# Optimization experiments

Hardware: AMD Instinct MI355X
Metric: run time of the kernel (lower is better)

## Reference

```python
import jax, jax.numpy as jnp
import numpy as np

N_INPUT, N_HIDDEN, N_OUTPUT = 64, 1024, 64
B, T = 128, 512

def setup_inputs() -> dict:
    key = jax.random.key(0)
    ks = jax.random.split(key, 8)
    s_in = 1.0 / np.sqrt(N_INPUT)
    s_h = 1.0 / np.sqrt(N_HIDDEN)
    return {
        "x": jax.random.normal(ks[0], (B, T, N_INPUT), jnp.float32),
        "enc_w": jax.random.uniform(ks[1], (N_HIDDEN, N_INPUT), jnp.float32, -s_in, s_in),
        "enc_b": jax.random.uniform(ks[2], (N_HIDDEN,), jnp.float32, -s_in, s_in),
        "rec_w": jax.random.uniform(ks[3], (N_HIDDEN, N_HIDDEN), jnp.float32, -s_h, s_h),
        "fgt_w": jax.random.uniform(ks[4], (N_HIDDEN, N_HIDDEN), jnp.float32, -s_h, s_h),
        "dec_w": jax.random.uniform(ks[5], (N_OUTPUT, N_HIDDEN), jnp.float32, -s_h, s_h),
        "dec_b": jax.random.uniform(ks[6], (N_OUTPUT,), jnp.float32, -s_h, s_h),
        "hinit_w": jax.random.uniform(ks[7], (N_HIDDEN, 1), jnp.float32, -1.0, 1.0),
        "hinit_b": jax.random.uniform(jax.random.fold_in(key, 9), (N_HIDDEN,), jnp.float32, -1.0, 1.0),
    }

def softsign(x):
    return x / (1.0 + jnp.abs(x))

def reference(x, enc_w, enc_b, rec_w, fgt_w, dec_w, dec_b, hinit_w, hinit_b):
    # x: [B, T, I] -> time-major [T, B, I]
    xt = jnp.transpose(x, (1, 0, 2))
    # hidden_init(ones(B,1)) = ones @ hinit_w^T + b = broadcast of column sum
    hidden0 = jnp.broadcast_to(hinit_w[:, 0] + hinit_b, (x.shape[0], hinit_b.shape[0]))
    # Precompute encoder projection for all timesteps (same math, one big GEMM)
    enc_all = jnp.einsum('tbi,hi->tbh', xt, enc_w) + enc_b  # [T, B, H]

    def step(hidden, enc_t):
        forget = jax.nn.sigmoid(hidden @ fgt_w.T)
        hidden_new = softsign(enc_t + hidden @ rec_w.T)
        hidden = (1.0 - forget) * hidden + forget * hidden_new
        out_t = hidden @ dec_w.T + dec_b
        return hidden, out_t

    hidden, output = jax.lax.scan(step, hidden0, enc_all)
    return output, hidden  # output: [T, B, O], hidden: [B, H]
```

## Files before the change

### kernel.cpp

```cpp
#include <hip/hip_runtime.h>

typedef unsigned short u16;

#define NWG 256
#define NT  256
#define TS  512
#define HD  1024
#define BS  128
#define NI  64
#define NO  64
#define XR  16
#define CC  32
#define RCP 17

typedef __attribute__((ext_vector_type(8))) short bf16x8;
typedef __attribute__((ext_vector_type(4))) float f32x4;

__device__ __forceinline__ float bf2f(u16 u) {
    union { unsigned int i; float f; } v; v.i = ((unsigned int)u) << 16; return v.f;
}
__device__ __forceinline__ u16 f2bf(float f) {
    union { float fl; unsigned int i; } v; v.fl = f;
    unsigned int x = v.i;
    return (u16)((x + 0x7fffu + ((x >> 16) & 1u)) >> 16);
}
__device__ __forceinline__ float ldv(const void* p, size_t i, bool isf32) {
    return isf32 ? ((const float*)p)[i] : bf2f(((const u16*)p)[i]);
}

__device__ __forceinline__ unsigned l2_atomic_add(unsigned* p, unsigned v) {
    unsigned old;
    asm volatile("global_atomic_add %0, %1, %2, off sc0\n\t"
                 "s_waitcnt vmcnt(0)"
                 : "=&v"(old) : "v"(p), "v"(v) : "memory");
    return old;
}
__device__ __forceinline__ void l2_atomic_swap_nr(unsigned* p, unsigned v) {
    asm volatile("global_atomic_swap %0, %1, off" :: "v"(p), "v"(v) : "memory");
}

__device__ __forceinline__ void load_a_frags(const u16* ap, bf16x8* a) {
    asm volatile(
        "global_load_dwordx4 %0, %8, off sc0\n\t"
        "global_load_dwordx4 %1, %8, off offset:64 sc0\n\t"
        "global_load_dwordx4 %2, %8, off offset:128 sc0\n\t"
        "global_load_dwordx4 %3, %8, off offset:192 sc0\n\t"
        "global_load_dwordx4 %4, %8, off offset:256 sc0\n\t"
        "global_load_dwordx4 %5, %8, off offset:320 sc0\n\t"
        "global_load_dwordx4 %6, %8, off offset:384 sc0\n\t"
        "global_load_dwordx4 %7, %8, off offset:448 sc0\n\t"
        "s_waitcnt vmcnt(0)"
        : "=&v"(a[0]), "=&v"(a[1]), "=&v"(a[2]), "=&v"(a[3]),
          "=&v"(a[4]), "=&v"(a[5]), "=&v"(a[6]), "=&v"(a[7])
        : "v"(ap) : "memory");
}

#define MBL 16

__global__ __launch_bounds__(NT)
void arnn_xcd(const void* __restrict__ xv,
              const void* __restrict__ encwv,
              const void* __restrict__ encbv,
              const void* __restrict__ recwv,
              const void* __restrict__ fgtwv,
              const void* __restrict__ decwv,
              const void* __restrict__ decbv,
              const void* __restrict__ hinitwv,
              const void* __restrict__ hinitbv,
              void* __restrict__ outv,
              u16* __restrict__ h0buf,
              u16* __restrict__ h1buf,
              unsigned* __restrict__ tickets,
              unsigned* __restrict__ mboxes)
{
    __shared__ short WB[132 * 64 * 8];
    __shared__ float redC[4 * 5 * 16 * RCP];
    __shared__ unsigned s_xcd, s_slot;
    __shared__ int s_f32;

    const int tid  = threadIdx.x;
    const int wave = tid >> 6;
    const int lane = tid & 63;
    const int m    = lane & 15;
    const int quad = lane >> 4;

    if (tid == 0) {
        unsigned xcc;
        asm volatile("s_getreg_b32 %0, hwreg(HW_REG_XCC_ID, 0, 4)" : "=s"(xcc));
        xcc &= 7u;
        unsigned slot = l2_atomic_add(tickets + xcc * 16, 1u);
        s_xcd = xcc;
        s_slot = slot & 31u;
        s_f32 = 0;
    }
    __syncthreads();
    {
        float v = bf2f(((const u16*)recwv)[tid]);
        if (!(v >= -1.0f && v <= 1.0f)) s_f32 = 1;
    }
    __syncthreads();
    const bool isf32 = (s_f32 != 0);
    const int xcd  = (int)s_xcd;
    const int slot = (int)s_slot;
    const int b0   = xcd * XR;
    const int j0   = slot * CC;
    const int dt   = slot & 3;
    const int rg   = slot >> 2;
    unsigned* mbX   = mboxes + (size_t)xcd * 32 * 4 * MBL;
    unsigned* mbW   = mbX + (slot * 4 + wave) * MBL;
    const int pw = (slot >> 3), pi = (slot & 7);

    for (int idx = tid; idx < 132 * 64; idx += NT) {
        int ksg = idx >> 6, l = idx & 63, n = l & 15, q = l >> 4;
        int tile, ksl;
        if (ksg < 34)       { tile = 0; ksl = ksg; }
        else if (ksg < 68)  { tile = 1; ksl = ksg - 34; }
        else if (ksg < 100) { tile = 2; ksl = ksg - 68; }
        else                { tile = 3; ksl = ksg - 100; }
        int j = j0 + ((tile & 1) << 4) + n;
        bf16x8 v;
        if (!isf32) {
            const u16* src;
            if (tile < 2) src = (ksl < 32) ? (const u16*)recwv + (size_t)j * HD + ksl * 32 + q * 8
                                           : (const u16*)encwv + (size_t)j * NI + (ksl - 32) * 32 + q * 8;
            else          src = (const u16*)fgtwv + (size_t)j * HD + ksl * 32 + q * 8;
            v = *(const bf16x8*)src;
        } else {
            const float* src;
            if (tile < 2) src = (ksl < 32) ? (const float*)recwv + (size_t)j * HD + ksl * 32 + q * 8
                                           : (const float*)encwv + (size_t)j * NI + (ksl - 32) * 32 + q * 8;
            else          src = (const float*)fgtwv + (size_t)j * HD + ksl * 32 + q * 8;
            #pragma unroll
            for (int i = 0; i < 8; ++i) v[i] = (short)f2bf(src[i]);
        }
        *(bf16x8*)&WB[idx * 8] = v;
    }
    __syncthreads();

    bf16x8 Breg[2][8];
    bf16x8 Freg[2][8];
    #pragma unroll
    for (int ks = 0; ks < 8; ++ks) {
        int kb = wave * 8 + ks;
        Breg[0][ks] = *(const bf16x8*)&WB[((0   + kb) * 64 + lane) * 8];
        Breg[1][ks] = *(const bf16x8*)&WB[((34  + kb) * 64 + lane) * 8];
        Freg[0][ks] = *(const bf16x8*)&WB[((68  + kb) * 64 + lane) * 8];
        Freg[1][ks] = *(const bf16x8*)&WB[((100 + kb) * 64 + lane) * 8];
    }
    bf16x8 Ereg[2];
    if (wave < 2) {
        Ereg[0] = *(const bf16x8*)&WB[((32 + wave) * 64 + lane) * 8];
        Ereg[1] = *(const bf16x8*)&WB[((34 + 32 + wave) * 64 + lane) * 8];
    }
    bf16x8 dfr[8];
    {
        int o = 16 * dt + m;
        #pragma unroll
        for (int ks = 0; ks < 8; ++ks) {
            int kb = wave * 256 + ks * 32 + quad * 8;
            if (!isf32) dfr[ks] = *(const bf16x8*)((const u16*)decwv + (size_t)o * HD + kb);
            else {
                const float* src = (const float*)decwv + (size_t)o * HD + kb;
                #pragma unroll
                for (int i = 0; i < 8; ++i) dfr[ks][i] = (short)f2bf(src[i]);
            }
        }
    }
    const int er2 = tid >> 4, ec2 = (tid & 15) * 2;
    float encb0 = ldv(encbv, j0 + ec2,     isf32);
    float encb1 = ldv(encbv, j0 + ec2 + 1, isf32);
    float decb_r = ldv(decbv, 16 * dt + (tid & 15), isf32);
    float hstA = ldv(hinitwv, j0 + ec2,     isf32) + ldv(hinitbv, j0 + ec2,     isf32);
    float hstB = ldv(hinitwv, j0 + ec2 + 1, isf32) + ldv(hinitbv, j0 + ec2 + 1, isf32);
    {
        unsigned pack = (unsigned)f2bf(hstA) | ((unsigned)f2bf(hstB) << 16);
        *(unsigned*)&h0buf[(size_t)(b0 + er2) * HD + j0 + ec2] = pack;
    }
    __syncthreads();
    if (tid < 32)
        l2_atomic_swap_nr(mbX + (tid * 4 + pw) * MBL + pi, 1u);

    bf16x8 xpB = {};
    f32x4 xr0 = {}, xr1 = {};
    if (wave < 2) {
        size_t xb = (size_t)(b0 + m) * (TS * NI) + (size_t)0 * NI + wave * 32 + quad * 8;
        if (!isf32) xpB = *(const bf16x8*)((const u16*)xv + xb);
        else { const float* xp = (const float*)xv + xb;
               xr0 = *(const f32x4*)xp; xr1 = *(const f32x4*)(xp + 4); }
    }

    for (int t = 0; t < TS; ++t) {
        f32x4 acc[5];
        #pragma unroll
        for (int tt = 0; tt < 5; ++tt) acc[tt] = (f32x4){0.f, 0.f, 0.f, 0.f};

        if (wave < 2) {
            bf16x8 xf;
            if (!isf32) xf = xpB;
            else {
                #pragma unroll
                for (int i = 0; i < 4; ++i) {
                    xf[i]     = (short)f2bf(xr0[i]);
                    xf[i + 4] = (short)f2bf(xr1[i]);
                }
            }
            acc[0] = __builtin_amdgcn_mfma_f32_16x16x32_bf16(xf, Ereg[0], acc[0], 0, 0, 0);
            acc[1] = __builtin_amdgcn_mfma_f32_16x16x32_bf16(xf, Ereg[1], acc[1], 0, 0, 0);
        }

        {
            const unsigned target = (unsigned)(t + 1);
            for (;;) {
                unsigned v = target;
                if (lane < 8) v = l2_atomic_add(mbW + lane, 0u);
                if (__all((int)(v >= target))) break;
            }
        }

        const u16* cur = (t & 1) ? h1buf : h0buf;
        u16*       nxt = (t & 1) ? h0buf : h1buf;

        bf16x8 a[8];
        load_a_frags(cur + (size_t)(b0 + m) * HD + wave * 256 + quad * 8, a);

        if (wave < 2) {
            int tn = (t + 1 < TS) ? t + 1 : t;
            size_t xb = (size_t)(b0 + m) * (TS * NI) + (size_t)tn * NI + wave * 32 + quad * 8;
            if (!isf32) xpB = *(const bf16x8*)((const u16*)xv + xb);
            else { const float* xp = (const float*)xv + xb;
                   xr0 = *(const f32x4*)xp; xr1 = *(const f32x4*)(xp + 4); }
        }

        #pragma unroll
        for (int ks = 0; ks < 8; ++ks) {
            acc[0] = __builtin_amdgcn_mfma_f32_16x16x32_bf16(a[ks], Breg[0][ks], acc[0], 0, 0, 0);
            acc[1] = __builtin_amdgcn_mfma_f32_16x16x32_bf16(a[ks], Breg[1][ks], acc[1], 0, 0, 0);
            acc[2] = __builtin_amdgcn_mfma_f32_16x16x32_bf16(a[ks], Freg[0][ks], acc[2], 0, 0, 0);
            acc[3] = __builtin_amdgcn_mfma_f32_16x16x32_bf16(a[ks], Freg[1][ks], acc[3], 0, 0, 0);
            acc[4] = __builtin_amdgcn_mfma_f32_16x16x32_bf16(a[ks], dfr[ks],     acc[4], 0, 0, 0);
        }

        #pragma unroll
        for (int tt = 0; tt < 5; ++tt) {
            #pragma unroll
            for (int r = 0; r < 4; ++r)
                redC[((wave * 5 + tt) * 16 + quad * 4 + r) * RCP + m] = acc[tt][r];
        }
        __syncthreads();

        {
            const int tl = ec2 >> 4, c0 = ec2 & 15;
            float pr0 = encb0, pf0 = 0.f, pr1 = encb1, pf1 = 0.f;
            #pragma unroll
            for (int kq = 0; kq < 4; ++kq) {
                pr0 += redC[((kq * 5 + tl) * 16 + er2) * RCP + c0];
                pf0 += redC[((kq * 5 + 2 + tl) * 16 + er2) * RCP + c0];
                pr1 += redC[((kq * 5 + tl) * 16 + er2) * RCP + c0 + 1];
                pf1 += redC[((kq * 5 + 2 + tl) * 16 + er2) * RCP + c0 + 1];
            }
            float fg0 = 1.0f / (1.0f + __expf(-pf0));
            float hn0 = pr0 / (1.0f + fabsf(pr0));
            hstA = hstA + fg0 * (hn0 - hstA);
            float fg1 = 1.0f / (1.0f + __expf(-pf1));
            float hn1 = pr1 / (1.0f + fabsf(pr1));
            hstB = hstB + fg1 * (hn1 - hstB);
            unsigned pack = (unsigned)f2bf(hstA) | ((unsigned)f2bf(hstB) << 16);
            *(unsigned*)&nxt[(size_t)(b0 + er2) * HD + j0 + ec2] = pack;
        }
        float dec_o = 0.f;
        int dr = 0;
        if (tid < 32) {
            dr = 2 * rg + (tid >> 4);
            int col = tid & 15;
            dec_o = decb_r;
            #pragma unroll
            for (int kq = 0; kq < 4; ++kq)
                dec_o += redC[((kq * 5 + 4) * 16 + dr) * RCP + col];
        }
        __syncthreads();
        if (tid < 32)
            l2_atomic_swap_nr(mbX + (tid * 4 + pw) * MBL + pi, (unsigned)(t + 2));
        if (tid < 32 && t > 0) {
            size_t oi = (size_t)(t - 1) * (BS * NO) + (size_t)(b0 + dr) * NO + 16 * dt + (tid & 15);
            if (isf32) ((float*)outv)[oi] = dec_o; else ((u16*)outv)[oi] = f2bf(dec_o);
        }
    }

    {
        {
            const unsigned target = (unsigned)(TS + 1);
            for (;;) {
                unsigned v = target;
                if (lane < 8) v = l2_atomic_add(mbW + lane, 0u);
                if (__all((int)(v >= target))) break;
            }
        }
        bf16x8 a[8];
        load_a_frags(h0buf + (size_t)(b0 + m) * HD + wave * 256 + quad * 8, a);
        f32x4 ac = (f32x4){0.f, 0.f, 0.f, 0.f};
        #pragma unroll
        for (int ks = 0; ks < 8; ++ks)
            ac = __builtin_amdgcn_mfma_f32_16x16x32_bf16(a[ks], dfr[ks], ac, 0, 0, 0);
        #pragma unroll
        for (int r = 0; r < 4; ++r)
            redC[((wave * 5 + 4) * 16 + quad * 4 + r) * RCP + m] = ac[r];
        __syncthreads();
        if (tid < 32) {
            int dr = 2 * rg + (tid >> 4), col = tid & 15;
            float o = decb_r;
            #pragma unroll
            for (int kq = 0; kq < 4; ++kq)
                o += redC[((kq * 5 + 4) * 16 + dr) * RCP + col];
            size_t oi = (size_t)511 * (BS * NO) + (size_t)(b0 + dr) * NO + 16 * dt + col;
            if (isf32) ((float*)outv)[oi] = o; else ((u16*)outv)[oi] = f2bf(o);
        }
    }
    {
        size_t oi = (size_t)TS * BS * NO + (size_t)(b0 + er2) * HD + j0 + ec2;
        if (isf32) { ((float*)outv)[oi] = hstA; ((float*)outv)[oi + 1] = hstB; }
        else {
            unsigned pack = (unsigned)f2bf(hstA) | ((unsigned)f2bf(hstB) << 16);
            *(unsigned*)&((u16*)outv)[oi] = pack;
        }
    }
}

extern "C" void kernel_launch(void* const* d_in, const int* in_sizes, int n_in,
                              void* d_out, int out_size, void* d_ws, size_t ws_size,
                              hipStream_t stream) {
    (void)in_sizes; (void)n_in; (void)out_size; (void)ws_size;
    const void* xv       = d_in[0];
    const void* encwv    = d_in[1];
    const void* encbv    = d_in[2];
    const void* recwv    = d_in[3];
    const void* fgtwv    = d_in[4];
    const void* decwv    = d_in[5];
    const void* decbv    = d_in[6];
    const void* hinitwv  = d_in[7];
    const void* hinitbv  = d_in[8];
    void* outv = d_out;

    unsigned* tickets = (unsigned*)d_ws;
    unsigned* mboxes  = (unsigned*)((char*)d_ws + 4096);
    u16* h0buf = (u16*)((char*)d_ws + 524288);
    u16* h1buf = h0buf + (size_t)BS * HD;

    hipMemsetAsync(d_ws, 0, 4096 + 8 * 32 * 4 * MBL * 4, stream);

    void* args[] = { (void*)&xv, (void*)&encwv, (void*)&encbv, (void*)&recwv,
                     (void*)&fgtwv, (void*)&decwv, (void*)&decbv,
                     (void*)&hinitwv, (void*)&hinitbv,
                     (void*)&outv, (void*)&h0buf, (void*)&h1buf,
                     (void*)&tickets, (void*)&mboxes };
    hipError_t err = hipLaunchCooperativeKernel((void*)arnn_xcd, dim3(NWG), dim3(NT), args, 0, stream);
    if (err != hipSuccess) {
        hipLaunchKernelGGL(arnn_xcd, dim3(NWG), dim3(NT), 0, stream,
                           xv, encwv, encbv, recwv, fgtwv, decwv, decbv,
                           hinitwv, hinitbv, outv, h0buf, h1buf, tickets, mboxes);
    }
}
```

Baseline: 1.435 ms.

## Double-buffer reduction scratch and signal per-wave mailboxes to drop a block barrier

The LDS reduction buffer is now double-buffered by timestep parity. This lets the end-of-step __syncthreads before the mailbox publish be removed. Each wave now publishes its own mailbox flag right after its stores drain (waitcnt vmcnt(0)), and pollers check 32 per-wave flags instead of 8. The weight staging area in LDS is halved by loading the recurrent and forget weights in two sequential phases, which frees space for the second reduction buffer. This cuts one block-wide barrier per timestep from the critical path of the cross-workgroup recurrence. The cost is more atomic traffic per publish and per poll, and it relies on per-wave store ordering for correctness.

```diff
diff --git a/kernel.cpp b/kernel.cpp
--- a/kernel.cpp
+++ b/kernel.cpp
@@ -12,6 +12,7 @@
 #define XR  16
 #define CC  32
 #define RCP 17
+#define MBW2 32
 
 typedef __attribute__((ext_vector_type(8))) short bf16x8;
 typedef __attribute__((ext_vector_type(4))) float f32x4;
@@ -55,7 +56,6 @@
         : "v"(ap) : "memory");
 }
 
-#define MBL 16
 
 __global__ __launch_bounds__(NT)
 void arnn_xcd(const void* __restrict__ xv,
@@ -73,8 +73,8 @@
               unsigned* __restrict__ tickets,
               unsigned* __restrict__ mboxes)
 {
-    __shared__ short WB[132 * 64 * 8];
-    __shared__ float redC[4 * 5 * 16 * RCP];
+    __shared__ short WB[68 * 64 * 8];
+    __shared__ float redC[2][4 * 5 * 16 * RCP];
     __shared__ unsigned s_xcd, s_slot;
     __shared__ int s_f32;
 
@@ -106,30 +106,23 @@
     const int j0   = slot * CC;
     const int dt   = slot & 3;
     const int rg   = slot >> 2;
-    unsigned* mbX   = mboxes + (size_t)xcd * 32 * 4 * MBL;
-    unsigned* mbW   = mbX + (slot * 4 + wave) * MBL;
+    unsigned* mbX = mboxes + (size_t)xcd * 32 * 4 * MBW2;
+    unsigned* mbW = mbX + (slot * 4 + wave) * MBW2;
     const int pw = (slot >> 3), pi = (slot & 7);
 
-    for (int idx = tid; idx < 132 * 64; idx += NT) {
+    for (int idx = tid; idx < 68 * 64; idx += NT) {
         int ksg = idx >> 6, l = idx & 63, n = l & 15, q = l >> 4;
-        int tile, ksl;
-        if (ksg < 34)       { tile = 0; ksl = ksg; }
-        else if (ksg < 68)  { tile = 1; ksl = ksg - 34; }
-        else if (ksg < 100) { tile = 2; ksl = ksg - 68; }
-        else                { tile = 3; ksl = ksg - 100; }
-        int j = j0 + ((tile & 1) << 4) + n;
+        int tile = (ksg < 34) ? 0 : 1;
+        int ksl  = ksg - 34 * tile;
+        int j = j0 + (tile << 4) + n;
         bf16x8 v;
         if (!isf32) {
-            const u16* src;
-            if (tile < 2) src = (ksl < 32) ? (const u16*)recwv + (size_t)j * HD + ksl * 32 + q * 8
-                                           : (const u16*)encwv + (size_t)j * NI + (ksl - 32) * 32 + q * 8;
-            else          src = (const u16*)fgtwv + (size_t)j * HD + ksl * 32 + q * 8;
+            const u16* src = (ksl < 32) ? (const u16*)recwv + (size_t)j * HD + ksl * 32 + q * 8
+                                        : (const u16*)encwv + (size_t)j * NI + (ksl - 32) * 32 + q * 8;
             v = *(const bf16x8*)src;
         } else {
-            const float* src;
-            if (tile < 2) src = (ksl < 32) ? (const float*)recwv + (size_t)j * HD + ksl * 32 + q * 8
-                                           : (const float*)encwv + (size_t)j * NI + (ksl - 32) * 32 + q * 8;
-            else          src = (const float*)fgtwv + (size_t)j * HD + ksl * 32 + q * 8;
+            const float* src = (ksl < 32) ? (const float*)recwv + (size_t)j * HD + ksl * 32 + q * 8
+                                          : (const float*)encwv + (size_t)j * NI + (ksl - 32) * 32 + q * 8;
             #pragma unroll
             for (int i = 0; i < 8; ++i) v[i] = (short)f2bf(src[i]);
         }
@@ -138,20 +131,44 @@
     __syncthreads();
 
     bf16x8 Breg[2][8];
+    #pragma unroll
+    for (int ks = 0; ks < 8; ++ks) {
+        int kb = wave * 8 + ks;
+        Breg[0][ks] = *(const bf16x8*)&WB[((0  + kb) * 64 + lane) * 8];
+        Breg[1][ks] = *(const bf16x8*)&WB[((34 + kb) * 64 + lane) * 8];
+    }
+    bf16x8 Ereg[2];
+    if (wave < 2) {
+        Ereg[0] = *(const bf16x8*)&WB[((32 + wave) * 64 + lane) * 8];
+        Ereg[1] = *(const bf16x8*)&WB[((34 + 32 + wave) * 64 + lane) * 8];
+    }
+    __syncthreads();
+
+    for (int idx = tid; idx < 64 * 64; idx += NT) {
+        int ksg = idx >> 6, l = idx & 63, n = l & 15, q = l >> 4;
+        int tile = ksg >> 5;
+        int ksl  = ksg & 31;
+        int j = j0 + (tile << 4) + n;
+        bf16x8 v;
+        if (!isf32) {
+            v = *(const bf16x8*)((const u16*)fgtwv + (size_t)j * HD + ksl * 32 + q * 8);
+        } else {
+            const float* src = (const float*)fgtwv + (size_t)j * HD + ksl * 32 + q * 8;
+            #pragma unroll
+            for (int i = 0; i < 8; ++i) v[i] = (short)f2bf(src[i]);
+        }
+        *(bf16x8*)&WB[idx * 8] = v;
+    }
+    __syncthreads();
+
     bf16x8 Freg[2][8];
     #pragma unroll
     for (int ks = 0; ks < 8; ++ks) {
         int kb = wave * 8 + ks;
-        Breg[0][ks] = *(const bf16x8*)&WB[((0   + kb) * 64 + lane) * 8];
-        Breg[1][ks] = *(const bf16x8*)&WB[((34  + kb) * 64 + lane) * 8];
-        Freg[0][ks] = *(const bf16x8*)&WB[((68  + kb) * 64 + lane) * 8];
-        Freg[1][ks] = *(const bf16x8*)&WB[((100 + kb) * 64 + lane) * 8];
-    }
-    bf16x8 Ereg[2];
-    if (wave < 2) {
-        Ereg[0] = *(const bf16x8*)&WB[((32 + wave) * 64 + lane) * 8];
-        Ereg[1] = *(const bf16x8*)&WB[((34 + 32 + wave) * 64 + lane) * 8];
-    }
+        Freg[0][ks] = *(const bf16x8*)&WB[((0  + kb) * 64 + lane) * 8];
+        Freg[1][ks] = *(const bf16x8*)&WB[((32 + kb) * 64 + lane) * 8];
+    }
+
     bf16x8 dfr[8];
     {
         int o = 16 * dt + m;
@@ -176,20 +193,21 @@
         unsigned pack = (unsigned)f2bf(hstA) | ((unsigned)f2bf(hstB) << 16);
         *(unsigned*)&h0buf[(size_t)(b0 + er2) * HD + j0 + ec2] = pack;
     }
-    __syncthreads();
-    if (tid < 32)
-        l2_atomic_swap_nr(mbX + (tid * 4 + pw) * MBL + pi, 1u);
+    asm volatile("s_waitcnt vmcnt(0)" ::: "memory");
+    if (lane < 32)
+        l2_atomic_swap_nr(mbX + (lane * 4 + pw) * MBW2 + pi * 4 + wave, 1u);
 
     bf16x8 xpB = {};
     f32x4 xr0 = {}, xr1 = {};
     if (wave < 2) {
-        size_t xb = (size_t)(b0 + m) * (TS * NI) + (size_t)0 * NI + wave * 32 + quad * 8;
+        size_t xb = (size_t)(b0 + m) * (TS * NI) + 0 * NI + wave * 32 + quad * 8;
         if (!isf32) xpB = *(const bf16x8*)((const u16*)xv + xb);
         else { const float* xp = (const float*)xv + xb;
                xr0 = *(const f32x4*)xp; xr1 = *(const f32x4*)(xp + 4); }
     }
 
     for (int t = 0; t < TS; ++t) {
+        float* rc = redC[t & 1];
         f32x4 acc[5];
         #pragma unroll
         for (int tt = 0; tt < 5; ++tt) acc[tt] = (f32x4){0.f, 0.f, 0.f, 0.f};
@@ -212,7 +230,7 @@
             const unsigned target = (unsigned)(t + 1);
             for (;;) {
                 unsigned v = target;
-                if (lane < 8) v = l2_atomic_add(mbW + lane, 0u);
+                if (lane < 32) v = l2_atomic_add(mbW + lane, 0u);
                 if (__all((int)(v >= target))) break;
             }
         }
@@ -244,7 +262,7 @@
         for (int tt = 0; tt < 5; ++tt) {
             #pragma unroll
             for (int r = 0; r < 4; ++r)
-                redC[((wave * 5 + tt) * 16 + quad * 4 + r) * RCP + m] = acc[tt][r];
+                rc[((wave * 5 + tt) * 16 + quad * 4 + r) * RCP + m] = acc[tt][r];
         }
         __syncthreads();
 
@@ -253,10 +271,10 @@
             float pr0 = encb0, pf0 = 0.f, pr1 = encb1, pf1 = 0.f;
             #pragma unroll
             for (int kq = 0; kq < 4; ++kq) {
-                pr0 += redC[((kq * 5 + tl) * 16 + er2) * RCP + c0];
-                pf0 += redC[((kq * 5 + 2 + tl) * 16 + er2) * RCP + c0];
-                pr1 += redC[((kq * 5 + tl) * 16 + er2) * RCP + c0 + 1];
-                pf1 += redC[((kq * 5 + 2 + tl) * 16 + er2) * RCP + c0 + 1];
+                pr0 += rc[((kq * 5 + tl) * 16 + er2) * RCP + c0];
+                pf0 += rc[((kq * 5 + 2 + tl) * 16 + er2) * RCP + c0];
+                pr1 += rc[((kq * 5 + tl) * 16 + er2) * RCP + c0 + 1];
+                pf1 += rc[((kq * 5 + 2 + tl) * 16 + er2) * RCP + c0 + 1];
             }
             float fg0 = 1.0f / (1.0f + __expf(-pf0));
             float hn0 = pr0 / (1.0f + fabsf(pr0));
@@ -267,22 +285,18 @@
             unsigned pack = (unsigned)f2bf(hstA) | ((unsigned)f2bf(hstB) << 16);
             *(unsigned*)&nxt[(size_t)(b0 + er2) * HD + j0 + ec2] = pack;
         }
-        float dec_o = 0.f;
-        int dr = 0;
-        if (tid < 32) {
-            dr = 2 * rg + (tid >> 4);
-            int col = tid & 15;
-            dec_o = decb_r;
+        asm volatile("s_waitcnt vmcnt(0)" ::: "memory");
+        if (lane < 32)
+            l2_atomic_swap_nr(mbX + (lane * 4 + pw) * MBW2 + pi * 4 + wave, (unsigned)(t + 2));
+
+        if (tid < 32 && t > 0) {
+            int dr = 2 * rg + (tid >> 4), col = tid & 15;
+            float o = decb_r;
             #pragma unroll
             for (int kq = 0; kq < 4; ++kq)
-                dec_o += redC[((kq * 5 + 4) * 16 + dr) * RCP + col];
-        }
-        __syncthreads();
-        if (tid < 32)
-            l2_atomic_swap_nr(mbX + (tid * 4 + pw) * MBL + pi, (unsigned)(t + 2));
-        if (tid < 32 && t > 0) {
-            size_t oi = (size_t)(t - 1) * (BS * NO) + (size_t)(b0 + dr) * NO + 16 * dt + (tid & 15);
-            if (isf32) ((float*)outv)[oi] = dec_o; else ((u16*)outv)[oi] = f2bf(dec_o);
+                o += rc[((kq * 5 + 4) * 16 + dr) * RCP + col];
+            size_t oi = (size_t)(t - 1) * (BS * NO) + (size_t)(b0 + dr) * NO + 16 * dt + col;
+            if (isf32) ((float*)outv)[oi] = o; else ((u16*)outv)[oi] = f2bf(o);
         }
     }
 
@@ -291,10 +305,11 @@
             const unsigned target = (unsigned)(TS + 1);
             for (;;) {
                 unsigned v = target;
-                if (lane < 8) v = l2_atomic_add(mbW + lane, 0u);
+                if (lane < 32) v = l2_atomic_add(mbW + lane, 0u);
                 if (__all((int)(v >= target))) break;
             }
         }
+        float* rc = redC[0];
         bf16x8 a[8];
         load_a_frags(h0buf + (size_t)(b0 + m) * HD + wave * 256 + quad * 8, a);
         f32x4 ac = (f32x4){0.f, 0.f, 0.f, 0.f};
@@ -303,14 +318,14 @@
             ac = __builtin_amdgcn_mfma_f32_16x16x32_bf16(a[ks], dfr[ks], ac, 0, 0, 0);
         #pragma unroll
         for (int r = 0; r < 4; ++r)
-            redC[((wave * 5 + 4) * 16 + quad * 4 + r) * RCP + m] = ac[r];
+            rc[((wave * 5 + 4) * 16 + quad * 4 + r) * RCP + m] = ac[r];
         __syncthreads();
         if (tid < 32) {
             int dr = 2 * rg + (tid >> 4), col = tid & 15;
             float o = decb_r;
             #pragma unroll
             for (int kq = 0; kq < 4; ++kq)
-                o += redC[((kq * 5 + 4) * 16 + dr) * RCP + col];
+                o += rc[((kq * 5 + 4) * 16 + dr) * RCP + col];
             size_t oi = (size_t)511 * (BS * NO) + (size_t)(b0 + dr) * NO + 16 * dt + col;
             if (isf32) ((float*)outv)[oi] = o; else ((u16*)outv)[oi] = f2bf(o);
         }
@@ -345,7 +360,7 @@
     u16* h0buf = (u16*)((char*)d_ws + 524288);
     u16* h1buf = h0buf + (size_t)BS * HD;
 
-    hipMemsetAsync(d_ws, 0, 4096 + 8 * 32 * 4 * MBL * 4, stream);
+    hipMemsetAsync(d_ws, 0, 4096 + 8 * 32 * 4 * MBW2 * 4, stream);
 
     void* args[] = { (void*)&xv, (void*)&encwv, (void*)&encbv, (void*)&recwv,
                      (void*)&fgtwv, (void*)&decwv, (void*)&decbv,
```

Measured after the change: 1.667 ms. 16.2% more time.
